# Optimization experiments

Hardware: AMD Instinct MI355X
Metric: run time of the kernel (lower is better)

Reference implementation:

```python
import jax, jax.numpy as jnp
import numpy as np

N_NODES = 10000
N_EDGES = 640000
D_IN = 128
D_OUT = 128


def setup_inputs() -> dict:
    key = jax.random.key(0)
    k1, k2, k3, k4 = jax.random.split(key, 4)
    nodes = jax.random.normal(k1, (N_NODES, D_IN), dtype=jnp.float32)
    senders = jax.random.randint(k2, (N_EDGES,), 0, N_NODES, dtype=jnp.int32)
    receivers = jax.random.randint(k3, (N_EDGES,), 0, N_NODES, dtype=jnp.int32)
    W = jax.random.normal(k4, (D_IN, D_OUT), dtype=jnp.float32) / np.sqrt(D_IN)
    b = jnp.zeros((D_OUT,), dtype=jnp.float32)
    return {"nodes": nodes, "senders": senders, "receivers": receivers, "W": W, "b": b}


def reference(nodes, senders, receivers, W, b):
    # gather messages from sender nodes: [E, D_IN]
    messages = nodes[senders]
    # scatter-add into receiver nodes: [N, D_IN]
    aggregated = jax.ops.segment_sum(messages, receivers, num_segments=nodes.shape[0])
    # in-degree per receiver node: [N]
    ones = jnp.ones((senders.shape[0],), dtype=nodes.dtype)
    degree = jax.ops.segment_sum(ones, receivers, num_segments=nodes.shape[0])
    degree = jnp.maximum(degree, 1.0)
    aggregated = aggregated / degree[:, None]
    # linear projection: [N, D_OUT]
    new_nodes = aggregated @ W + b
    return new_nodes
```

## Files before the change

### kernel.cpp

```cpp
#include <hip/hip_runtime.h>

#define N_NODES 10000
#define N_EDGES 640000
#define D       128

#define GEMM_BLOCKS 313
#define HB          64
#define CHUNK       10000
#define PAD         256
#define GROUPS      8
#define NODES_PER_GROUP 1250
#define SBPG        128

__device__ inline unsigned bf16pair(float a, float b) {
    unsigned ua = __float_as_uint(a), ub = __float_as_uint(b);
    ua = (ua + 0x7fffu + ((ua >> 16) & 1u)) >> 16;
    ub = (ub + 0x7fffu + ((ub >> 16) & 1u)) >> 16;
    return ua | (ub << 16);
}

union FusedSmem {
    float As[32][132];
    int   cnt[N_NODES];
};

__global__ __launch_bounds__(256) void gemm_hist_kernel(const float* __restrict__ nodes,
                                                        const float* __restrict__ Wm,
                                                        unsigned* __restrict__ Yb,
                                                        const int* __restrict__ senders,
                                                        const int* __restrict__ receivers,
                                                        unsigned* __restrict__ pack,
                                                        int* __restrict__ bcnt) {
    __shared__ FusedSmem sm;
    const int t = threadIdx.x;

    if (blockIdx.x < GEMM_BLOCKS) {
        const int row0 = blockIdx.x * 32;

        for (int i = t; i < 1024; i += 256) {
            int r  = i >> 5;
            int c  = i & 31;
            int gr = row0 + r;
            float4 v = make_float4(0.f, 0.f, 0.f, 0.f);
            if (gr < N_NODES) v = ((const float4*)nodes)[gr * 32 + c];
            *((float4*)&sm.As[r][c * 4]) = v;
        }
        __syncthreads();

        const int tx = t & 15;
        const int ty = t >> 4;
        const int c0 = tx * 8;
        const int r0 = ty * 2;

        float acc[2][8];
#pragma unroll
        for (int i = 0; i < 2; i++)
#pragma unroll
            for (int j = 0; j < 8; j++) acc[i][j] = 0.f;

        const float4* W4 = (const float4*)Wm;
#pragma unroll 4
        for (int k = 0; k < 128; k++) {
            float  a0 = sm.As[r0][k];
            float  a1 = sm.As[r0 + 1][k];
            float4 w0 = W4[k * 32 + tx * 2];
            float4 w1 = W4[k * 32 + tx * 2 + 1];
            float  wv[8] = {w0.x, w0.y, w0.z, w0.w, w1.x, w1.y, w1.z, w1.w};
#pragma unroll
            for (int j = 0; j < 8; j++) {
                acc[0][j] += a0 * wv[j];
                acc[1][j] += a1 * wv[j];
            }
        }

#pragma unroll
        for (int i = 0; i < 2; i++) {
            int gr = row0 + r0 + i;
            if (gr < N_NODES) {
                uint4 o;
                o.x = bf16pair(acc[i][0], acc[i][1]);
                o.y = bf16pair(acc[i][2], acc[i][3]);
                o.z = bf16pair(acc[i][4], acc[i][5]);
                o.w = bf16pair(acc[i][6], acc[i][7]);
                ((uint4*)Yb)[gr * 16 + (c0 >> 3)] = o;
            }
        }
    } else {
        const int b = blockIdx.x - GEMM_BLOCKS;
        for (int n = t; n < N_NODES; n += 256) sm.cnt[n] = 0;
        __syncthreads();
        const int base = b * CHUNK;
        for (int i = t; i < CHUNK; i += 256) {
            int r = receivers[base + i];
            int s = senders[base + i];
            int l = atomicAdd(&sm.cnt[r], 1);
            pack[base + i] = (unsigned)s | ((unsigned)r << 14) | ((unsigned)l << 28);
        }
        __syncthreads();
        int* dst = bcnt + b * N_NODES;
        for (int n = t; n < N_NODES; n += 256) dst[n] = sm.cnt[n];
    }
}

__global__ __launch_bounds__(256) void colscan_kernel(int* __restrict__ bcnt,
                                                      int* __restrict__ deg) {
    const int g = blockIdx.x * 256 + threadIdx.x;
    const int n = g >> 2;
    const int q = g & 3;
    if (n >= N_NODES) return;

    int pre[16];
    int s = 0;
#pragma unroll
    for (int j = 0; j < 16; j++) {
        int v = bcnt[(q * 16 + j) * N_NODES + n];
        pre[j] = s;
        s += v;
    }

    const int lane = threadIdx.x & 63;
    const int gb   = lane & ~3;
    int s0 = __shfl(s, gb + 0);
    int s1 = __shfl(s, gb + 1);
    int s2 = __shfl(s, gb + 2);
    int off = (q > 0 ? s0 : 0) + (q > 1 ? s1 : 0) + (q > 2 ? s2 : 0);

#pragma unroll
    for (int j = 0; j < 16; j++)
        bcnt[(q * 16 + j) * N_NODES + n] = off + pre[j];
    if (q == 3) deg[n] = off + s;
}

__global__ __launch_bounds__(256) void scatter_kernel(const unsigned* __restrict__ pack,
                                                      const int* __restrict__ bcnt,
                                                      int* __restrict__ csr) {
    const int x  = blockIdx.x & 7;
    const int bg = blockIdx.x >> 3;
    const int lo = x * NODES_PER_GROUP;
    const int hi = lo + NODES_PER_GROUP;

    for (int i = bg * 256 + threadIdx.x; i < N_EDGES / 4; i += SBPG * 256) {
        int b = i / (CHUNK / 4);
        const int* pre = bcnt + b * N_NODES;
        uint4 p = ((const uint4*)pack)[i];
#pragma unroll
        for (int q = 0; q < 4; q++) {
            unsigned wd = (q == 0) ? p.x : (q == 1) ? p.y : (q == 2) ? p.z : p.w;
            int r = (int)((wd >> 14) & 0x3fffu);
            if (r >= lo && r < hi) {
                int s = (int)(wd & 0x3fffu);
                int l = (int)(wd >> 28);
                csr[(r << 8) + pre[r] + l] = s;
            }
        }
    }
}

__global__ __launch_bounds__(128) void gather_kernel(const unsigned* __restrict__ Yb,
                                                     const int* __restrict__ deg,
                                                     const int* __restrict__ csr,
                                                     const float* __restrict__ bias,
                                                     float* __restrict__ out) {
    const int t  = threadIdx.x;
    const int d4 = t & 15;
    const int ep = t >> 4;

    __shared__ int   lds_s[PAD];
    __shared__ float red[8][128];

#pragma unroll
    for (int nn = 0; nn < 2; nn++) {
        const int n   = blockIdx.x * 2 + nn;
        const int dg  = deg[n];
        const int lim = min(dg, PAD);

        for (int i = t; i < lim; i += 128) lds_s[i] = csr[(n << 8) + i];
        __syncthreads();

        float acc[8];
#pragma unroll
        for (int k = 0; k < 8; k++) acc[k] = 0.f;

        for (int j = ep; j < lim; j += 8) {
            int   s = lds_s[j];
            uint4 v = ((const uint4*)Yb)[s * 16 + d4];
            acc[0] += __uint_as_float(v.x << 16);
            acc[1] += __uint_as_float(v.x & 0xffff0000u);
            acc[2] += __uint_as_float(v.y << 16);
            acc[3] += __uint_as_float(v.y & 0xffff0000u);
            acc[4] += __uint_as_float(v.z << 16);
            acc[5] += __uint_as_float(v.z & 0xffff0000u);
            acc[6] += __uint_as_float(v.w << 16);
            acc[7] += __uint_as_float(v.w & 0xffff0000u);
        }

        ((float4*)&red[ep][d4 * 8])[0] = make_float4(acc[0], acc[1], acc[2], acc[3]);
        ((float4*)&red[ep][d4 * 8])[1] = make_float4(acc[4], acc[5], acc[6], acc[7]);
        __syncthreads();

        float sum = 0.f;
#pragma unroll
        for (int e = 0; e < 8; e++) sum += red[e][t];
        float inv = 1.0f / (float)max(dg, 1);
        out[n * 128 + t] = sum * inv + bias[t];
        __syncthreads();
    }
}

extern "C" void kernel_launch(void* const* d_in, const int* in_sizes, int n_in,
                              void* d_out, int out_size, void* d_ws, size_t ws_size,
                              hipStream_t stream) {
    const float* nodes     = (const float*)d_in[0];
    const int*   senders   = (const int*)  d_in[1];
    const int*   receivers = (const int*)  d_in[2];
    const float* Wm        = (const float*)d_in[3];
    const float* bias      = (const float*)d_in[4];
    float*       out       = (float*)d_out;

    char*     w    = (char*)d_ws;
    unsigned* Yb   = (unsigned*)(w);
    unsigned* pack = (unsigned*)(w + 2560000);
    int*      bcnt = (int*)(w + 5120000);
    int*      deg  = (int*)(w + 7680000);
    int*      csr  = (int*)(w + 7720448);

    gemm_hist_kernel<<<GEMM_BLOCKS + HB, 256, 0, stream>>>(nodes, Wm, Yb,
                                                           senders, receivers,
                                                           pack, bcnt);
    colscan_kernel  <<<(4 * N_NODES + 255) / 256, 256, 0, stream>>>(bcnt, deg);
    scatter_kernel  <<<GROUPS * SBPG, 256, 0, stream>>>(pack, bcnt, csr);
    gather_kernel   <<<N_NODES / 2, 128, 0, stream>>>(Yb, deg, csr, bias, out);
}
```

Before: 111.0 us.

## Replace histogram/scan/scatter CSR build with global atomic cursor slots

Removes the per-chunk LDS histogram, the column prefix scan and the separate scatter kernel. Edges are now bucketed by having each one claim a slot in a fixed 256-wide per-node row through a global atomicAdd on a cursor array. The scatter runs alongside the GEMM blocks in one launch, and the cursor doubles as the degree. This cuts two kernel launches and the pack/bcnt traffic, at the cost of contended global atomics and a memset. The order of senders inside each row becomes nondeterministic, so float summation order can vary between runs.

```diff
diff --git a/kernel.cpp b/kernel.cpp
--- a/kernel.cpp
+++ b/kernel.cpp
@@ -5,12 +5,8 @@
 #define D       128
 
 #define GEMM_BLOCKS 313
-#define HB          64
-#define CHUNK       10000
+#define SCAT_BLOCKS 512
 #define PAD         256
-#define GROUPS      8
-#define NODES_PER_GROUP 1250
-#define SBPG        128
 
 __device__ inline unsigned bf16pair(float a, float b) {
     unsigned ua = __float_as_uint(a), ub = __float_as_uint(b);
@@ -19,19 +15,14 @@
     return ua | (ub << 16);
 }
 
-union FusedSmem {
-    float As[32][132];
-    int   cnt[N_NODES];
-};
-
-__global__ __launch_bounds__(256) void gemm_hist_kernel(const float* __restrict__ nodes,
-                                                        const float* __restrict__ Wm,
-                                                        unsigned* __restrict__ Yb,
-                                                        const int* __restrict__ senders,
-                                                        const int* __restrict__ receivers,
-                                                        unsigned* __restrict__ pack,
-                                                        int* __restrict__ bcnt) {
-    __shared__ FusedSmem sm;
+__global__ __launch_bounds__(256) void gemm_scatter_kernel(const float* __restrict__ nodes,
+                                                           const float* __restrict__ Wm,
+                                                           unsigned* __restrict__ Yb,
+                                                           const int* __restrict__ senders,
+                                                           const int* __restrict__ receivers,
+                                                           int* __restrict__ cursor,
+                                                           int* __restrict__ csr) {
+    __shared__ float As[32][132];
     const int t = threadIdx.x;
 
     if (blockIdx.x < GEMM_BLOCKS) {
@@ -43,7 +34,7 @@
             int gr = row0 + r;
             float4 v = make_float4(0.f, 0.f, 0.f, 0.f);
             if (gr < N_NODES) v = ((const float4*)nodes)[gr * 32 + c];
-            *((float4*)&sm.As[r][c * 4]) = v;
+            *((float4*)&As[r][c * 4]) = v;
         }
         __syncthreads();
 
@@ -61,8 +52,8 @@
         const float4* W4 = (const float4*)Wm;
 #pragma unroll 4
         for (int k = 0; k < 128; k++) {
-            float  a0 = sm.As[r0][k];
-            float  a1 = sm.As[r0 + 1][k];
+            float  a0 = As[r0][k];
+            float  a1 = As[r0 + 1][k];
             float4 w0 = W4[k * 32 + tx * 2];
             float4 w1 = W4[k * 32 + tx * 2 + 1];
             float  wv[8] = {w0.x, w0.y, w0.z, w0.w, w1.x, w1.y, w1.z, w1.w};
@@ -86,72 +77,20 @@
             }
         }
     } else {
-        const int b = blockIdx.x - GEMM_BLOCKS;
-        for (int n = t; n < N_NODES; n += 256) sm.cnt[n] = 0;
-        __syncthreads();
-        const int base = b * CHUNK;
-        for (int i = t; i < CHUNK; i += 256) {
-            int r = receivers[base + i];
-            int s = senders[base + i];
-            int l = atomicAdd(&sm.cnt[r], 1);
-            pack[base + i] = (unsigned)s | ((unsigned)r << 14) | ((unsigned)l << 28);
-        }
-        __syncthreads();
-        int* dst = bcnt + b * N_NODES;
-        for (int n = t; n < N_NODES; n += 256) dst[n] = sm.cnt[n];
-    }
-}
-
-__global__ __launch_bounds__(256) void colscan_kernel(int* __restrict__ bcnt,
-                                                      int* __restrict__ deg) {
-    const int g = blockIdx.x * 256 + threadIdx.x;
-    const int n = g >> 2;
-    const int q = g & 3;
-    if (n >= N_NODES) return;
-
-    int pre[16];
-    int s = 0;
-#pragma unroll
-    for (int j = 0; j < 16; j++) {
-        int v = bcnt[(q * 16 + j) * N_NODES + n];
-        pre[j] = s;
-        s += v;
-    }
-
-    const int lane = threadIdx.x & 63;
-    const int gb   = lane & ~3;
-    int s0 = __shfl(s, gb + 0);
-    int s1 = __shfl(s, gb + 1);
-    int s2 = __shfl(s, gb + 2);
-    int off = (q > 0 ? s0 : 0) + (q > 1 ? s1 : 0) + (q > 2 ? s2 : 0);
-
-#pragma unroll
-    for (int j = 0; j < 16; j++)
-        bcnt[(q * 16 + j) * N_NODES + n] = off + pre[j];
-    if (q == 3) deg[n] = off + s;
-}
-
-__global__ __launch_bounds__(256) void scatter_kernel(const unsigned* __restrict__ pack,
-                                                      const int* __restrict__ bcnt,
-                                                      int* __restrict__ csr) {
-    const int x  = blockIdx.x & 7;
-    const int bg = blockIdx.x >> 3;
-    const int lo = x * NODES_PER_GROUP;
-    const int hi = lo + NODES_PER_GROUP;
-
-    for (int i = bg * 256 + threadIdx.x; i < N_EDGES / 4; i += SBPG * 256) {
-        int b = i / (CHUNK / 4);
-        const int* pre = bcnt + b * N_NODES;
-        uint4 p = ((const uint4*)pack)[i];
-#pragma unroll
-        for (int q = 0; q < 4; q++) {
-            unsigned wd = (q == 0) ? p.x : (q == 1) ? p.y : (q == 2) ? p.z : p.w;
-            int r = (int)((wd >> 14) & 0x3fffu);
-            if (r >= lo && r < hi) {
-                int s = (int)(wd & 0x3fffu);
-                int l = (int)(wd >> 28);
-                csr[(r << 8) + pre[r] + l] = s;
-            }
+        const int  b  = blockIdx.x - GEMM_BLOCKS;
+        const int4* s4 = (const int4*)senders;
+        const int4* r4 = (const int4*)receivers;
+        for (int i = b * 256 + t; i < N_EDGES / 4; i += SCAT_BLOCKS * 256) {
+            int4 s = s4[i];
+            int4 r = r4[i];
+            int p0 = atomicAdd(&cursor[r.x], 1);
+            int p1 = atomicAdd(&cursor[r.y], 1);
+            int p2 = atomicAdd(&cursor[r.z], 1);
+            int p3 = atomicAdd(&cursor[r.w], 1);
+            csr[(r.x << 8) + p0] = s.x;
+            csr[(r.y << 8) + p1] = s.y;
+            csr[(r.z << 8) + p2] = s.z;
+            csr[(r.w << 8) + p3] = s.w;
         }
     }
 }
@@ -217,17 +156,13 @@
     const float* bias      = (const float*)d_in[4];
     float*       out       = (float*)d_out;
 
-    char*     w    = (char*)d_ws;
-    unsigned* Yb   = (unsigned*)(w);
-    unsigned* pack = (unsigned*)(w + 2560000);
-    int*      bcnt = (int*)(w + 5120000);
-    int*      deg  = (int*)(w + 7680000);
-    int*      csr  = (int*)(w + 7720448);
+    char* w      = (char*)d_ws;
+    unsigned* Yb = (unsigned*)(w);
+    int* cursor  = (int*)(w + 2560000);
+    int* csr     = (int*)(w + 2600192);
 
-    gemm_hist_kernel<<<GEMM_BLOCKS + HB, 256, 0, stream>>>(nodes, Wm, Yb,
-                                                           senders, receivers,
-                                                           pack, bcnt);
-    colscan_kernel  <<<(4 * N_NODES + 255) / 256, 256, 0, stream>>>(bcnt, deg);
-    scatter_kernel  <<<GROUPS * SBPG, 256, 0, stream>>>(pack, bcnt, csr);
-    gather_kernel   <<<N_NODES / 2, 128, 0, stream>>>(Yb, deg, csr, bias, out);
+    hipMemsetAsync(cursor, 0, N_NODES * sizeof(int), stream);
+    gemm_scatter_kernel<<<GEMM_BLOCKS + SCAT_BLOCKS, 256, 0, stream>>>(
+        nodes, Wm, Yb, senders, receivers, cursor, csr);
+    gather_kernel<<<N_NODES / 2, 128, 0, stream>>>(Yb, cursor, csr, bias, out);
 }
```

After: 138.1 us. 1.24x slower.

## Assign one node per 16-thread group in gather, removing LDS reduction and syncs

Applied to the files above, without the earlier changes.

The gather kernel now maps each node to a 16-lane group, and each lane walks the whole neighbour list for its 8 columns. Previously a 128-thread block split a node's edges across 8 lanes and combined them with an LDS reduction. The change also unrolls the neighbour loop by 4 so several independent row loads are in flight, and drops the shared-memory staging of CSR indices and all barriers. In exchange, each group serially walks about 64 edges, and lanes in a wavefront can diverge when node degrees differ. The 16 lanes of a group read the same CSR index, so that load is effectively a broadcast.

```diff
diff --git a/kernel.cpp b/kernel.cpp
--- a/kernel.cpp
+++ b/kernel.cpp
@@ -156,55 +156,65 @@
     }
 }
 
-__global__ __launch_bounds__(128) void gather_kernel(const unsigned* __restrict__ Yb,
+__device__ inline void acc8(float* acc, uint4 v) {
+    acc[0] += __uint_as_float(v.x << 16);
+    acc[1] += __uint_as_float(v.x & 0xffff0000u);
+    acc[2] += __uint_as_float(v.y << 16);
+    acc[3] += __uint_as_float(v.y & 0xffff0000u);
+    acc[4] += __uint_as_float(v.z << 16);
+    acc[5] += __uint_as_float(v.z & 0xffff0000u);
+    acc[6] += __uint_as_float(v.w << 16);
+    acc[7] += __uint_as_float(v.w & 0xffff0000u);
+}
+
+__global__ __launch_bounds__(256) void gather_kernel(const unsigned* __restrict__ Yb,
                                                      const int* __restrict__ deg,
                                                      const int* __restrict__ csr,
                                                      const float* __restrict__ bias,
                                                      float* __restrict__ out) {
     const int t  = threadIdx.x;
     const int d4 = t & 15;
-    const int ep = t >> 4;
-
-    __shared__ int   lds_s[PAD];
-    __shared__ float red[8][128];
-
-#pragma unroll
-    for (int nn = 0; nn < 2; nn++) {
-        const int n   = blockIdx.x * 2 + nn;
-        const int dg  = deg[n];
-        const int lim = min(dg, PAD);
-
-        for (int i = t; i < lim; i += 128) lds_s[i] = csr[(n << 8) + i];
-        __syncthreads();
-
-        float acc[8];
-#pragma unroll
-        for (int k = 0; k < 8; k++) acc[k] = 0.f;
-
-        for (int j = ep; j < lim; j += 8) {
-            int   s = lds_s[j];
-            uint4 v = ((const uint4*)Yb)[s * 16 + d4];
-            acc[0] += __uint_as_float(v.x << 16);
-            acc[1] += __uint_as_float(v.x & 0xffff0000u);
-            acc[2] += __uint_as_float(v.y << 16);
-            acc[3] += __uint_as_float(v.y & 0xffff0000u);
-            acc[4] += __uint_as_float(v.z << 16);
-            acc[5] += __uint_as_float(v.z & 0xffff0000u);
-            acc[6] += __uint_as_float(v.w << 16);
-            acc[7] += __uint_as_float(v.w & 0xffff0000u);
-        }
-
-        ((float4*)&red[ep][d4 * 8])[0] = make_float4(acc[0], acc[1], acc[2], acc[3]);
-        ((float4*)&red[ep][d4 * 8])[1] = make_float4(acc[4], acc[5], acc[6], acc[7]);
-        __syncthreads();
-
-        float sum = 0.f;
-#pragma unroll
-        for (int e = 0; e < 8; e++) sum += red[e][t];
-        float inv = 1.0f / (float)max(dg, 1);
-        out[n * 128 + t] = sum * inv + bias[t];
-        __syncthreads();
-    }
+    const int n  = blockIdx.x * 16 + (t >> 4);
+
+    const int dg   = deg[n];
+    const int lim  = min(dg, PAD);
+    const int base = n << 8;
+
+    float acc[8];
+#pragma unroll
+    for (int k = 0; k < 8; k++) acc[k] = 0.f;
+
+    const uint4* Y4 = (const uint4*)Yb;
+
+    int j = 0;
+    for (; j + 4 <= lim; j += 4) {
+        int s0 = csr[base + j];
+        int s1 = csr[base + j + 1];
+        int s2 = csr[base + j + 2];
+        int s3 = csr[base + j + 3];
+        uint4 v0 = Y4[s0 * 16 + d4];
+        uint4 v1 = Y4[s1 * 16 + d4];
+        uint4 v2 = Y4[s2 * 16 + d4];
+        uint4 v3 = Y4[s3 * 16 + d4];
+        acc8(acc, v0);
+        acc8(acc, v1);
+        acc8(acc, v2);
+        acc8(acc, v3);
+    }
+    for (; j < lim; j++) {
+        int s = csr[base + j];
+        acc8(acc, Y4[s * 16 + d4]);
+    }
+
+    const float inv = 1.0f / (float)max(dg, 1);
+    float4 b0 = ((const float4*)bias)[d4 * 2];
+    float4 b1 = ((const float4*)bias)[d4 * 2 + 1];
+    float4 o0 = make_float4(acc[0] * inv + b0.x, acc[1] * inv + b0.y,
+                            acc[2] * inv + b0.z, acc[3] * inv + b0.w);
+    float4 o1 = make_float4(acc[4] * inv + b1.x, acc[5] * inv + b1.y,
+                            acc[6] * inv + b1.z, acc[7] * inv + b1.w);
+    ((float4*)&out[n * 128 + d4 * 8])[0] = o0;
+    ((float4*)&out[n * 128 + d4 * 8])[1] = o1;
 }
 
 extern "C" void kernel_launch(void* const* d_in, const int* in_sizes, int n_in,
@@ -229,5 +239,5 @@
                                                            pack, bcnt);
     colscan_kernel  <<<(4 * N_NODES + 255) / 256, 256, 0, stream>>>(bcnt, deg);
     scatter_kernel  <<<GROUPS * SBPG, 256, 0, stream>>>(pack, bcnt, csr);
-    gather_kernel   <<<N_NODES / 2, 128, 0, stream>>>(Yb, deg, csr, bias, out);
-}
+    gather_kernel   <<<(N_NODES + 15) / 16, 256, 0, stream>>>(Yb, deg, csr, bias, out);
+}
```

Result: no change. 112.9 us (+1.8%).
